# Kernel tuning notes

Hardware: AMD Instinct MI355X
Metric: run time of the kernel (lower is better)

The kernel has to match this reference:

```python
import jax, jax.numpy as jnp
import numpy as np

B, C, HIMG, WIMG = 32, 3, 224, 224
P, D, L, F, H, NC = 16, 768, 12, 3072, 12, 1000
S = (HIMG // P) * (WIMG // P)  # 196 tokens
DH = D // H                    # 64 per head


def setup_inputs() -> dict:
    key = jax.random.key(0)
    ks = jax.random.split(key, 12)
    rn = lambda i, shape, sc: jax.random.normal(ks[i], shape, jnp.float32) * sc
    return dict(
        x=rn(0, (B, C, HIMG, WIMG), 1.0),
        conv_w=rn(1, (D, C, P, P), 0.02),
        conv_b=jnp.zeros((D,), jnp.float32),
        pos_embed=rn(2, (S, D), 0.02),
        ln1_s=jnp.ones((L, D), jnp.float32),
        ln1_b=jnp.zeros((L, D), jnp.float32),
        wq=rn(3, (L, D, D), 0.02),
        wk=rn(4, (L, D, D), 0.02),
        wv=rn(5, (L, D, D), 0.02),
        ln2_s=jnp.ones((L, D), jnp.float32),
        ln2_b=jnp.zeros((L, D), jnp.float32),
        w1=rn(6, (L, D, F), 0.02),
        b1=jnp.zeros((L, F), jnp.float32),
        w2=rn(7, (L, F, D), 0.02),
        b2=jnp.zeros((L, D), jnp.float32),
        fc_w=rn(8, (D, NC), 0.02),
        fc_b=jnp.zeros((NC,), jnp.float32),
    )


def _layernorm(x, scale, bias, eps=1e-5):
    m = x.mean(-1, keepdims=True)
    v = ((x - m) ** 2).mean(-1, keepdims=True)
    return (x - m) * jax.lax.rsqrt(v + eps) * scale + bias


def reference(x, conv_w, conv_b, pos_embed, ln1_s, ln1_b, wq, wk, wv,
              ln2_s, ln2_b, w1, b1, w2, b2, fc_w, fc_b):
    # patch embedding: stride-P conv, then b c h w -> b (h w) c, add pos embed
    h = jax.lax.conv_general_dilated(
        x, conv_w, (P, P), 'VALID',
        dimension_numbers=('NCHW', 'OIHW', 'NCHW'))
    h = h + conv_b[None, :, None, None]
    h = h.reshape(B, D, S).transpose(0, 2, 1) + pos_embed  # [B,S,D]

    # NOTE: original scales attention logits by 1/sqrt(seq_len), not 1/sqrt(d_head)
    scale = 1.0 / jnp.sqrt(jnp.float32(S))

    def layer(hx, p):
        l1s, l1b, Wq, Wk, Wv, l2s, l2b, W1, B1, W2, B2 = p
        xn = _layernorm(hx, l1s, l1b)
        q = (xn @ Wq).reshape(B, S, H, DH)
        k = (xn @ Wk).reshape(B, S, H, DH)
        v = (xn @ Wv).reshape(B, S, H, DH)
        att = jax.nn.softmax(jnp.einsum('bshd,bthd->bhst', q, k) * scale, axis=-1)
        o = jnp.einsum('bhst,bthd->bshd', att, v).reshape(B, S, D)
        hx = hx + o
        y = _layernorm(hx, l2s, l2b) @ W1 + B1
        y = jax.nn.gelu(y, approximate=False) @ W2 + B2
        return hx + y, None

    h, _ = jax.lax.scan(layer, h, (ln1_s, ln1_b, wq, wk, wv,
                                   ln2_s, ln2_b, w1, b1, w2, b2))
    return h.mean(axis=1) @ fc_w + fc_b  # [B, num_classes]
```

## Files before the change

kernel.cpp:

```cpp
#include <hip/hip_runtime.h>
#include <hip/hip_bf16.h>

typedef __attribute__((ext_vector_type(8))) short bf16x8;
typedef __attribute__((ext_vector_type(4))) short bf16x4;
typedef __attribute__((ext_vector_type(4))) float f32x4;

#define DEVI static __device__ __forceinline__

DEVI unsigned short f2bf(float f) {
  __hip_bfloat16 h = __float2bfloat16(f);
  return __builtin_bit_cast(unsigned short, h);
}

DEVI f32x4 mfma16(bf16x8 a, bf16x8 b, f32x4 c) {
  return __builtin_amdgcn_mfma_f32_16x16x32_bf16(a, b, c, 0, 0, 0);
}

DEVI void gload16(const unsigned short* g, unsigned short* l) {
  __builtin_amdgcn_global_load_lds(
      (const __attribute__((address_space(1))) void*)g,
      (__attribute__((address_space(3))) void*)l, 16, 0, 0);
}

DEVI float erf_fast(float x) {
  float ax = fabsf(x);
  float t = 1.f / (1.f + 0.3275911f * ax);
  float poly = ((((1.061405429f * t - 1.453152027f) * t + 1.421413741f) * t -
                 0.284496736f) * t + 0.254829592f) * t;
  float e = __expf(-x * x);
  float er = 1.f - poly * e;
  return copysignf(er, x);
}

__global__ __launch_bounds__(256) void k_im2col(const float* __restrict__ x,
                                                unsigned short* __restrict__ A) {
  int t = blockIdx.x * 256 + threadIdx.x;
  int m = t / 192;
  int qq = t - m * 192;
  int kk = qq * 4;
  int c = kk >> 8;
  int r = kk & 255;
  int i = r >> 4;
  int j = r & 15;
  int b = m / 196;
  int s = m - b * 196;
  int ph = s / 14;
  int pw = s - ph * 14;
  const float* src = x + ((size_t)((b * 3 + c) * 224 + ph * 16 + i)) * 224 + pw * 16 + j;
  f32x4 v = *reinterpret_cast<const f32x4*>(src);
  bf16x4 o;
  o[0] = (short)f2bf(v[0]); o[1] = (short)f2bf(v[1]);
  o[2] = (short)f2bf(v[2]); o[3] = (short)f2bf(v[3]);
  *reinterpret_cast<bf16x4*>(A + (size_t)m * 768 + kk) = o;
}

__global__ __launch_bounds__(256) void k_cvt(const float* __restrict__ in,
                                             unsigned short* __restrict__ out) {
  int t = blockIdx.x * 256 + threadIdx.x;
  f32x4 v = *reinterpret_cast<const f32x4*>(in + (size_t)t * 4);
  bf16x4 o;
  o[0] = (short)f2bf(v[0]); o[1] = (short)f2bf(v[1]);
  o[2] = (short)f2bf(v[2]); o[3] = (short)f2bf(v[3]);
  *reinterpret_cast<bf16x4*>(out + (size_t)t * 4) = o;
}

DEVI void transpose_tile(const float* __restrict__ in, unsigned short* __restrict__ out,
                         int K, int N, int kt, int nt, unsigned short (*tile)[68]) {
  int r = threadIdx.x >> 4;
  int c4 = (threadIdx.x & 15) * 4;
  int k0 = kt * 64, n0 = nt * 64;
#pragma unroll
  for (int rr0 = 0; rr0 < 4; rr0++) {
    int rr = r + rr0 * 16;
    f32x4 v = *reinterpret_cast<const f32x4*>(in + (size_t)(k0 + rr) * N + n0 + c4);
    bf16x4 o;
    o[0] = (short)f2bf(v[0]); o[1] = (short)f2bf(v[1]);
    o[2] = (short)f2bf(v[2]); o[3] = (short)f2bf(v[3]);
    *reinterpret_cast<bf16x4*>(&tile[rr][c4]) = o;
  }
  __syncthreads();
#pragma unroll
  for (int rr0 = 0; rr0 < 4; rr0++) {
    int rr = r + rr0 * 16;
    bf16x4 o;
    o[0] = (short)tile[c4 + 0][rr];
    o[1] = (short)tile[c4 + 1][rr];
    o[2] = (short)tile[c4 + 2][rr];
    o[3] = (short)tile[c4 + 3][rr];
    *reinterpret_cast<bf16x4*>(out + (size_t)(n0 + rr) * K + k0 + c4) = o;
  }
}

__global__ __launch_bounds__(256) void k_wconvert(
    const float* __restrict__ wq, const float* __restrict__ wk, const float* __restrict__ wv,
    const float* __restrict__ w1, const float* __restrict__ w2,
    unsigned short* __restrict__ wqkvT, unsigned short* __restrict__ w1T,
    unsigned short* __restrict__ w2T) {
  __shared__ unsigned short tile[64][68];
  int bid = blockIdx.x;
  if (bid < 432) {
    int mm = bid / 144, t2 = bid - mm * 144;
    const float* in = (mm == 0) ? wq : ((mm == 1) ? wk : wv);
    transpose_tile(in, wqkvT + (size_t)mm * 768 * 768, 768, 768, t2 / 12, t2 % 12, tile);
  } else if (bid < 1008) {
    int t2 = bid - 432;
    transpose_tile(w1, w1T, 768, 3072, t2 / 48, t2 % 48, tile);
  } else {
    int t2 = bid - 1008;
    transpose_tile(w2, w2T, 3072, 768, t2 / 12, t2 % 12, tile);
  }
}

__global__ __launch_bounds__(256) void k_ln(const float* __restrict__ h,
                                            const float* __restrict__ sc,
                                            const float* __restrict__ bi,
                                            unsigned short* __restrict__ xn) {
  int wave = threadIdx.x >> 6, lane = threadIdx.x & 63;
  int row = blockIdx.x * 4 + wave;
  const float* hr = h + (size_t)row * 768;
  f32x4 v[3];
  float sum = 0.f;
#pragma unroll
  for (int i = 0; i < 3; i++) {
    v[i] = *reinterpret_cast<const f32x4*>(hr + i * 256 + lane * 4);
    sum += v[i][0] + v[i][1] + v[i][2] + v[i][3];
  }
#pragma unroll
  for (int m = 1; m < 64; m <<= 1) sum += __shfl_xor(sum, m, 64);
  float mean = sum * (1.f / 768.f);
  float var = 0.f;
#pragma unroll
  for (int i = 0; i < 3; i++)
#pragma unroll
    for (int c = 0; c < 4; c++) { float d = v[i][c] - mean; var += d * d; }
#pragma unroll
  for (int m = 1; m < 64; m <<= 1) var += __shfl_xor(var, m, 64);
  float rs = rsqrtf(var * (1.f / 768.f) + 1e-5f);
#pragma unroll
  for (int i = 0; i < 3; i++) {
    int col = i * 256 + lane * 4;
    f32x4 s4 = *reinterpret_cast<const f32x4*>(sc + col);
    f32x4 b4 = *reinterpret_cast<const f32x4*>(bi + col);
    bf16x4 o;
#pragma unroll
    for (int c = 0; c < 4; c++) o[c] = (short)f2bf((v[i][c] - mean) * rs * s4[c] + b4[c]);
    *reinterpret_cast<bf16x4*>(xn + (size_t)row * 768 + col) = o;
  }
}

template <int EPI>
__global__ __launch_bounds__(256) void k_gemm(
    const unsigned short* __restrict__ A, const unsigned short* __restrict__ Bt, int K,
    const float* __restrict__ bias, const float* __restrict__ aux,
    float* __restrict__ outF, unsigned short* __restrict__ outB) {
  __shared__ __align__(16) unsigned short As[2][128 * 32];
  __shared__ __align__(16) unsigned short Bs[2][128 * 32];

  int GX = gridDim.x, GY = gridDim.y;
  int nb = GX * GY;
  int lin = blockIdx.y * GX + blockIdx.x;
  int q = nb >> 3, r8 = nb & 7;
  int xcd = lin & 7, off = lin >> 3;
  int wid = (xcd < r8 ? xcd * (q + 1) : r8 * (q + 1) + (xcd - r8) * q) + off;
  const int GM = 8;
  int per = GM * GX;
  int g = wid / per;
  int first_m = g * GM;
  int gm = min(GM, GY - first_m);
  int rem = wid - g * per;
  int mt = first_m + rem % gm;
  int nt = rem / gm;
  int m0 = mt * 128, n0 = nt * 128;

  int tid = threadIdx.x;
  int wave = tid >> 6, lane = tid & 63;
  int wm = (wave >> 1) * 64, wn = (wave & 1) * 64;
  int lr = lane & 15, lg = lane >> 4;

  f32x4 acc[4][4];
  const f32x4 fz = {0.f, 0.f, 0.f, 0.f};
#pragma unroll
  for (int i = 0; i < 4; i++)
#pragma unroll
    for (int j = 0; j < 4; j++) acc[i][j] = fz;

  int srow = wave * 16 + (lane >> 2);
  int scol = (lane & 3) * 8;
  const unsigned short* Ag = A + (size_t)(m0 + srow) * K + scol;
  const unsigned short* Bg = Bt + (size_t)(n0 + srow) * K + scol;
  int lofs = wave * 16 * 32;

  int nk = K >> 5;
#pragma unroll
  for (int j = 0; j < 2; j++) {
    gload16(Ag + (size_t)j * 64 * K, &As[0][lofs + j * 64 * 32]);
    gload16(Bg + (size_t)j * 64 * K, &Bs[0][lofs + j * 64 * 32]);
  }
  __syncthreads();

  for (int kt = 0; kt < nk - 1; kt++) {
    int cur = kt & 1;
    int k0 = (kt + 1) << 5;
#pragma unroll
    for (int j = 0; j < 2; j++) {
      gload16(Ag + (size_t)j * 64 * K + k0, &As[cur ^ 1][lofs + j * 64 * 32]);
      gload16(Bg + (size_t)j * 64 * K + k0, &Bs[cur ^ 1][lofs + j * 64 * 32]);
    }
    bf16x8 a[4], b[4];
#pragma unroll
    for (int i = 0; i < 4; i++) {
      a[i] = *reinterpret_cast<const bf16x8*>(&As[cur][(wm + i * 16 + lr) * 32 + lg * 8]);
      b[i] = *reinterpret_cast<const bf16x8*>(&Bs[cur][(wn + i * 16 + lr) * 32 + lg * 8]);
    }
#pragma unroll
    for (int mi = 0; mi < 4; mi++)
#pragma unroll
      for (int ni = 0; ni < 4; ni++) acc[mi][ni] = mfma16(a[mi], b[ni], acc[mi][ni]);
    __syncthreads();
  }
  {
    int cur = (nk - 1) & 1;
    bf16x8 a[4], b[4];
#pragma unroll
    for (int i = 0; i < 4; i++) {
      a[i] = *reinterpret_cast<const bf16x8*>(&As[cur][(wm + i * 16 + lr) * 32 + lg * 8]);
      b[i] = *reinterpret_cast<const bf16x8*>(&Bs[cur][(wn + i * 16 + lr) * 32 + lg * 8]);
    }
#pragma unroll
    for (int mi = 0; mi < 4; mi++)
#pragma unroll
      for (int ni = 0; ni < 4; ni++) acc[mi][ni] = mfma16(a[mi], b[ni], acc[mi][ni]);
  }

  if (EPI == 1) {
#pragma unroll
    for (int ni = 0; ni < 4; ni++) {
      int n = n0 + wn + ni * 16 + lr;
      int which = (n >= 1536) ? 2 : ((n >= 768) ? 1 : 0);
      int n7 = n - which * 768;
      int hd = n7 >> 6, dh = n7 & 63;
      unsigned short* ob = outB + (size_t)which * 4816896 + dh;
#pragma unroll
      for (int mi = 0; mi < 4; mi++) {
        int mb = m0 + wm + mi * 16 + lg * 4;
        int bb = mb / 196;
        int s = mb - bb * 196;
#pragma unroll
        for (int r = 0; r < 4; r++) {
          ob[((size_t)((bb * 12 + hd) * 196 + s) << 6)] = f2bf(acc[mi][ni][r]);
          s++;
          if (s == 196) { s = 0; bb++; }
        }
      }
    }
  } else {
#pragma unroll
    for (int mi = 0; mi < 4; mi++) {
      int mb = m0 + wm + mi * 16 + lg * 4;
      int bb = mb / 196;
      int s0 = mb - bb * 196;
#pragma unroll
      for (int ni = 0; ni < 4; ni++) {
        int n = n0 + wn + ni * 16 + lr;
        int s = s0;
#pragma unroll
        for (int r = 0; r < 4; r++) {
          int m = mb + r;
          float val = acc[mi][ni][r];
          if (EPI == 0) {
            outF[(size_t)m * 768 + n] = val + bias[n] + aux[(size_t)s * 768 + n];
            s++;
            if (s == 196) s = 0;
          } else if (EPI == 2) {
            float u = val + bias[n];
            float gg = 0.5f * u * (1.f + erf_fast(u * 0.70710678118654752f));
            outB[(size_t)m * 3072 + n] = f2bf(gg);
          } else {
            outF[(size_t)m * 768 + n] += val + bias[n];
          }
        }
      }
    }
  }
}

__global__ __launch_bounds__(256) void k_attn(const unsigned short* __restrict__ q,
                                              const unsigned short* __restrict__ k,
                                              const unsigned short* __restrict__ v,
                                              float* __restrict__ h) {
  __shared__ __align__(16) unsigned short Kl[208][72];
  __shared__ __align__(16) unsigned short Vt[64][248];
  __shared__ __align__(16) unsigned short Sc[4][16][232];
  int bh = blockIdx.x;
  int b = bh / 12, hh = bh - b * 12;
  size_t base = (size_t)bh * 196 * 64;
  int tid = threadIdx.x, wave = tid >> 6, lane = tid & 63;
  int lr = lane & 15, lg = lane >> 4;

  const bf16x8 bz = {0, 0, 0, 0, 0, 0, 0, 0};
  for (int u = tid; u < 208 * 8; u += 256) {
    int row = u >> 3, c8 = (u & 7) * 8;
    bf16x8 val = bz;
    if (row < 196) val = *reinterpret_cast<const bf16x8*>(k + base + row * 64 + c8);
    *reinterpret_cast<bf16x8*>(&Kl[row][c8]) = val;
  }
  for (int u = tid; u < 224 * 8; u += 256) {
    int t = u >> 3, d8 = (u & 7) * 8;
    bf16x8 val = bz;
    if (t < 196) val = *reinterpret_cast<const bf16x8*>(v + base + t * 64 + d8);
#pragma unroll
    for (int i = 0; i < 8; i++) Vt[d8 + i][t] = (unsigned short)val[i];
  }
  for (int i2 = lane; i2 < 256; i2 += 64) Sc[wave][i2 >> 4][208 + (i2 & 15)] = 0;
  __syncthreads();

  const float scale = 1.f / 14.f;
  for (int st = wave; st < 13; st += 4) {
    int qb = st * 16;
    int s = qb + lr;
    bf16x8 aq0 = bz, aq1 = bz;
    if (s < 196) {
      aq0 = *reinterpret_cast<const bf16x8*>(q + base + (size_t)s * 64 + lg * 8);
      aq1 = *reinterpret_cast<const bf16x8*>(q + base + (size_t)s * 64 + 32 + lg * 8);
    }
    f32x4 sc[13];
#pragma unroll
    for (int t = 0; t < 13; t++) {
      bf16x8 bk0 = *reinterpret_cast<const bf16x8*>(&Kl[t * 16 + lr][lg * 8]);
      bf16x8 bk1 = *reinterpret_cast<const bf16x8*>(&Kl[t * 16 + lr][32 + lg * 8]);
      f32x4 z = {0.f, 0.f, 0.f, 0.f};
      z = mfma16(aq0, bk0, z);
      z = mfma16(aq1, bk1, z);
      sc[t] = z;
    }
    float mx[4] = {-1e30f, -1e30f, -1e30f, -1e30f};
#pragma unroll
    for (int t = 0; t < 13; t++) {
      int tc = t * 16 + lr;
#pragma unroll
      for (int r = 0; r < 4; r++) {
        float xv = (tc < 196) ? sc[t][r] * scale : -1e30f;
        sc[t][r] = xv;
        mx[r] = fmaxf(mx[r], xv);
      }
    }
#pragma unroll
    for (int r = 0; r < 4; r++)
#pragma unroll
      for (int mm = 1; mm < 16; mm <<= 1) mx[r] = fmaxf(mx[r], __shfl_xor(mx[r], mm, 64));
    float sm[4] = {0.f, 0.f, 0.f, 0.f};
#pragma unroll
    for (int t = 0; t < 13; t++)
#pragma unroll
      for (int r = 0; r < 4; r++) {
        float e = __expf(sc[t][r] - mx[r]);
        sc[t][r] = e;
        sm[r] += e;
      }
#pragma unroll
    for (int r = 0; r < 4; r++)
#pragma unroll
      for (int mm = 1; mm < 16; mm <<= 1) sm[r] += __shfl_xor(sm[r], mm, 64);
    float inv[4];
#pragma unroll
    for (int r = 0; r < 4; r++) inv[r] = 1.f / sm[r];
#pragma unroll
    for (int t = 0; t < 13; t++)
#pragma unroll
      for (int r = 0; r < 4; r++)
        Sc[wave][lg * 4 + r][t * 16 + lr] = f2bf(sc[t][r] * inv[r]);
    asm volatile("s_waitcnt lgkmcnt(0)" ::: "memory");
    bf16x8 ap[7];
#pragma unroll
    for (int ks = 0; ks < 7; ks++)
      ap[ks] = *reinterpret_cast<const bf16x8*>(&Sc[wave][lr][ks * 32 + lg * 8]);
#pragma unroll
    for (int nt = 0; nt < 4; nt++) {
      f32x4 o = {0.f, 0.f, 0.f, 0.f};
#pragma unroll
      for (int ks = 0; ks < 7; ks++) {
        bf16x8 bv = *reinterpret_cast<const bf16x8*>(&Vt[nt * 16 + lr][ks * 32 + lg * 8]);
        o = mfma16(ap[ks], bv, o);
      }
#pragma unroll
      for (int r = 0; r < 4; r++) {
        int s2 = qb + lg * 4 + r;
        if (s2 < 196) h[(size_t)(b * 196 + s2) * 768 + hh * 64 + nt * 16 + lr] += o[r];
      }
    }
  }
}

__global__ __launch_bounds__(256) void k_mean(const float* __restrict__ h,
                                              float* __restrict__ hm) {
  int b = blockIdx.x, d = blockIdx.y * 256 + threadIdx.x;
  float acc = 0.f;
  for (int s = 0; s < 196; s++) acc += h[(size_t)(b * 196 + s) * 768 + d];
  hm[b * 768 + d] = acc * (1.f / 196.f);
}

__global__ __launch_bounds__(256) void k_fc(const float* __restrict__ hm,
                                            const float* __restrict__ w,
                                            const float* __restrict__ bias,
                                            float* __restrict__ out) {
  int b = blockIdx.x, n = blockIdx.y * 256 + threadIdx.x;
  if (n >= 1000) return;
  float acc = bias[n];
  for (int d = 0; d < 768; d++) acc += hm[b * 768 + d] * w[d * 1000 + n];
  out[b * 1000 + n] = acc;
}

extern "C" void kernel_launch(void* const* d_in, const int* in_sizes, int n_in,
                              void* d_out, int out_size, void* d_ws, size_t ws_size,
                              hipStream_t stream) {
  const float* x      = (const float*)d_in[0];
  const float* conv_w = (const float*)d_in[1];
  const float* conv_b = (const float*)d_in[2];
  const float* pos    = (const float*)d_in[3];
  const float* ln1_s  = (const float*)d_in[4];
  const float* ln1_b  = (const float*)d_in[5];
  const float* wq     = (const float*)d_in[6];
  const float* wk     = (const float*)d_in[7];
  const float* wv     = (const float*)d_in[8];
  const float* ln2_s  = (const float*)d_in[9];
  const float* ln2_b  = (const float*)d_in[10];
  const float* w1     = (const float*)d_in[11];
  const float* b1     = (const float*)d_in[12];
  const float* w2     = (const float*)d_in[13];
  const float* b2     = (const float*)d_in[14];
  const float* fc_w   = (const float*)d_in[15];
  const float* fc_b   = (const float*)d_in[16];
  float* out = (float*)d_out;

  char* p = (char*)d_ws;
  auto alloc = [&](size_t bytes) {
    char* r = p;
    p += (bytes + 255) & ~(size_t)255;
    return r;
  };
  const size_t M = 6272, QSZ = 4816896;
  float* h              = (float*)alloc(M * 768 * 4);
  unsigned short* xn    = (unsigned short*)alloc(M * 768 * 2);
  unsigned short* qkv   = (unsigned short*)alloc(3 * QSZ * 2);
  unsigned short* y1    = (unsigned short*)alloc(M * 3072 * 2);
  unsigned short* wqkvT = (unsigned short*)alloc((size_t)2304 * 768 * 2);
  unsigned short* w1T   = (unsigned short*)alloc((size_t)3072 * 768 * 2);
  unsigned short* w2T   = (unsigned short*)alloc((size_t)3072 * 768 * 2);
  unsigned short* cwB   = (unsigned short*)alloc((size_t)768 * 768 * 2);
  float* hm             = (float*)alloc(32 * 768 * 4);

  k_cvt<<<576, 256, 0, stream>>>(conv_w, cwB);
  k_im2col<<<4704, 256, 0, stream>>>(x, xn);
  k_gemm<0><<<dim3(6, 49), 256, 0, stream>>>(xn, cwB, 768, conv_b, pos, h, nullptr);

  for (int l = 0; l < 12; l++) {
    k_wconvert<<<1584, 256, 0, stream>>>(
        wq + (size_t)l * 589824, wk + (size_t)l * 589824, wv + (size_t)l * 589824,
        w1 + (size_t)l * 2359296, w2 + (size_t)l * 2359296, wqkvT, w1T, w2T);
    k_ln<<<1568, 256, 0, stream>>>(h, ln1_s + l * 768, ln1_b + l * 768, xn);
    k_gemm<1><<<dim3(18, 49), 256, 0, stream>>>(xn, wqkvT, 768, nullptr, nullptr, nullptr, qkv);
    k_attn<<<384, 256, 0, stream>>>(qkv, qkv + QSZ, qkv + 2 * QSZ, h);
    k_ln<<<1568, 256, 0, stream>>>(h, ln2_s + l * 768, ln2_b + l * 768, xn);
    k_gemm<2><<<dim3(24, 49), 256, 0, stream>>>(xn, w1T, 768, b1 + (size_t)l * 3072, nullptr,
                                                nullptr, y1);
    k_gemm<3><<<dim3(6, 49), 256, 0, stream>>>(y1, w2T, 3072, b2 + (size_t)l * 768, nullptr, h,
                                               nullptr);
  }
  k_mean<<<dim3(32, 3), 256, 0, stream>>>(h, hm);
  k_fc<<<dim3(32, 4), 256, 0, stream>>>(hm, fc_w, fc_b, out);
}
```

Before: 3.274 ms.

## Split-K the FC2 GEMM four ways with atomic accumulation into residual

```diff
diff --git a/kernel.cpp b/kernel.cpp
--- a/kernel.cpp
+++ b/kernel.cpp
@@ -151,26 +151,30 @@
 template <int EPI>
 __global__ __launch_bounds__(256) void k_gemm(
     const unsigned short* __restrict__ A, const unsigned short* __restrict__ Bt, int K,
-    const float* __restrict__ bias, const float* __restrict__ aux,
+    int nks, const float* __restrict__ bias, const float* __restrict__ aux,
     float* __restrict__ outF, unsigned short* __restrict__ outB) {
   __shared__ __align__(16) unsigned short As[2][128 * 32];
   __shared__ __align__(16) unsigned short Bs[2][128 * 32];
 
-  int GX = gridDim.x, GY = gridDim.y;
-  int nb = GX * GY;
-  int lin = blockIdx.y * GX + blockIdx.x;
+  int GX = gridDim.x, GY = gridDim.y, GZ = gridDim.z;
+  int nb = GX * GY * GZ;
+  int lin = (blockIdx.z * GY + blockIdx.y) * GX + blockIdx.x;
   int q = nb >> 3, r8 = nb & 7;
   int xcd = lin & 7, off = lin >> 3;
   int wid = (xcd < r8 ? xcd * (q + 1) : r8 * (q + 1) + (xcd - r8) * q) + off;
+  int t2 = GX * GY;
+  int sz = wid / t2;
+  int w2 = wid - sz * t2;
   const int GM = 8;
   int per = GM * GX;
-  int g = wid / per;
+  int g = w2 / per;
   int first_m = g * GM;
   int gm = min(GM, GY - first_m);
-  int rem = wid - g * per;
+  int rem = w2 - g * per;
   int mt = first_m + rem % gm;
   int nt = rem / gm;
   int m0 = mt * 128, n0 = nt * 128;
+  int kb = sz * nks * 32;
 
   int tid = threadIdx.x;
   int wave = tid >> 6, lane = tid & 63;
@@ -186,11 +190,10 @@
 
   int srow = wave * 16 + (lane >> 2);
   int scol = (lane & 3) * 8;
-  const unsigned short* Ag = A + (size_t)(m0 + srow) * K + scol;
-  const unsigned short* Bg = Bt + (size_t)(n0 + srow) * K + scol;
+  const unsigned short* Ag = A + (size_t)(m0 + srow) * K + scol + kb;
+  const unsigned short* Bg = Bt + (size_t)(n0 + srow) * K + scol + kb;
   int lofs = wave * 16 * 32;
 
-  int nk = K >> 5;
 #pragma unroll
   for (int j = 0; j < 2; j++) {
     gload16(Ag + (size_t)j * 64 * K, &As[0][lofs + j * 64 * 32]);
@@ -198,7 +201,7 @@
   }
   __syncthreads();
 
-  for (int kt = 0; kt < nk - 1; kt++) {
+  for (int kt = 0; kt < nks - 1; kt++) {
     int cur = kt & 1;
     int k0 = (kt + 1) << 5;
 #pragma unroll
@@ -219,7 +222,7 @@
     __syncthreads();
   }
   {
-    int cur = (nk - 1) & 1;
+    int cur = (nks - 1) & 1;
     bf16x8 a[4], b[4];
 #pragma unroll
     for (int i = 0; i < 4; i++) {
@@ -276,7 +279,8 @@
             float gg = 0.5f * u * (1.f + erf_fast(u * 0.70710678118654752f));
             outB[(size_t)m * 3072 + n] = f2bf(gg);
           } else {
-            outF[(size_t)m * 768 + n] += val + bias[n];
+            float bn = (sz == 0) ? bias[n] : 0.f;
+            atomicAdd(&outF[(size_t)m * 768 + n], val + bn);
           }
         }
       }
@@ -438,33 +442,34 @@
     p += (bytes + 255) & ~(size_t)255;
     return r;
   };
-  const size_t M = 6272, QSZ = 4816896;
+  const size_t M = 6272, MP = 6400, QSZ = 4816896;
   float* h              = (float*)alloc(M * 768 * 4);
-  unsigned short* xn    = (unsigned short*)alloc(M * 768 * 2);
+  unsigned short* xn    = (unsigned short*)alloc(MP * 768 * 2);
   unsigned short* qkv   = (unsigned short*)alloc(3 * QSZ * 2);
-  unsigned short* y1    = (unsigned short*)alloc(M * 3072 * 2);
+  unsigned short* y1    = (unsigned short*)alloc(MP * 3072 * 2);
   unsigned short* wqkvT = (unsigned short*)alloc((size_t)2304 * 768 * 2);
   unsigned short* w1T   = (unsigned short*)alloc((size_t)3072 * 768 * 2);
   unsigned short* w2T   = (unsigned short*)alloc((size_t)3072 * 768 * 2);
-  unsigned short* cwB   = (unsigned short*)alloc((size_t)768 * 768 * 2);
   float* hm             = (float*)alloc(32 * 768 * 4);
+  unsigned short* cwB   = qkv;
 
   k_cvt<<<576, 256, 0, stream>>>(conv_w, cwB);
   k_im2col<<<4704, 256, 0, stream>>>(x, xn);
-  k_gemm<0><<<dim3(6, 49), 256, 0, stream>>>(xn, cwB, 768, conv_b, pos, h, nullptr);
+  k_gemm<0><<<dim3(6, 49, 1), 256, 0, stream>>>(xn, cwB, 768, 24, conv_b, pos, h, nullptr);
 
   for (int l = 0; l < 12; l++) {
     k_wconvert<<<1584, 256, 0, stream>>>(
         wq + (size_t)l * 589824, wk + (size_t)l * 589824, wv + (size_t)l * 589824,
         w1 + (size_t)l * 2359296, w2 + (size_t)l * 2359296, wqkvT, w1T, w2T);
     k_ln<<<1568, 256, 0, stream>>>(h, ln1_s + l * 768, ln1_b + l * 768, xn);
-    k_gemm<1><<<dim3(18, 49), 256, 0, stream>>>(xn, wqkvT, 768, nullptr, nullptr, nullptr, qkv);
+    k_gemm<1><<<dim3(18, 49, 1), 256, 0, stream>>>(xn, wqkvT, 768, 24, nullptr, nullptr,
+                                                   nullptr, qkv);
     k_attn<<<384, 256, 0, stream>>>(qkv, qkv + QSZ, qkv + 2 * QSZ, h);
     k_ln<<<1568, 256, 0, stream>>>(h, ln2_s + l * 768, ln2_b + l * 768, xn);
-    k_gemm<2><<<dim3(24, 49), 256, 0, stream>>>(xn, w1T, 768, b1 + (size_t)l * 3072, nullptr,
-                                                nullptr, y1);
-    k_gemm<3><<<dim3(6, 49), 256, 0, stream>>>(y1, w2T, 3072, b2 + (size_t)l * 768, nullptr, h,
-                                               nullptr);
+    k_gemm<2><<<dim3(24, 49, 1), 256, 0, stream>>>(xn, w1T, 768, 24, b1 + (size_t)l * 3072,
+                                                   nullptr, nullptr, y1);
+    k_gemm<3><<<dim3(6, 49, 4), 256, 0, stream>>>(y1, w2T, 3072, 24, b2 + (size_t)l * 768,
+                                                  nullptr, h, nullptr);
   }
   k_mean<<<dim3(32, 3), 256, 0, stream>>>(h, hm);
   k_fc<<<dim3(32, 4), 256, 0, stream>>>(hm, fc_w, fc_b, out);
```

Result: slower. 3.610 ms (+10.3%).
